# Optimization experiments

Measured on AMD Instinct MI355X. Metric: run time of the kernel, lower is better.

The kernel has to match this reference:

```python
import jax, jax.numpy as jnp
import numpy as np

TIME_SHIFT_OFFSET = 288
NOTE_OFF_OFFSET = 128
VELOCITY_OFFSET = 256
MAX_REL_POS = 25
MAX_REL_TIME = 200
MAX_REL_PITCH = 128


def _last_true_pos(flag):
    # flag: (B,T) bool -> (B,T) index of most recent True at or before each position, -1 if none
    B, T = flag.shape
    pos = jnp.where(flag, jnp.arange(T)[None, :], -1)
    return jax.lax.cummax(pos, axis=1)


def time_rel_idx(tok):
    # Faithful vectorization of Head.relative_time index computation.
    B, T = tok.shape
    is_t = tok >= TIME_SHIFT_OFFSET
    vals = jnp.where(is_t, tok - TIME_SHIFT_OFFSET, 0)
    abs_t = (jnp.cumsum(vals, axis=1) + 1).astype(jnp.float32)
    last = _last_true_pos(is_t)
    cur = jnp.where(last >= 0, jnp.take_along_axis(abs_t, jnp.maximum(last, 0), axis=1), jnp.nan)
    prop = jnp.round(cur / 10.0)  # (B,T), NaN before first time token
    dist = prop[:, None, :] - prop[:, :, None]  # [b,i,j] = prop[j]-prop[i]
    idx = jnp.clip(dist, -MAX_REL_TIME, MAX_REL_TIME) + MAX_REL_TIME
    return jnp.where(jnp.isnan(idx), 0.0, idx).astype(jnp.int32)  # (B,T,T)


def pitch_rel_idx(tok):
    # Per the reference loop, note values are also written one step ahead (i-1,i,i+1),
    # so position j ends up with the note value known after step min(j+1, T-1).
    B, T = tok.shape
    is_n = tok < VELOCITY_OFFSET
    vals = (jnp.where(tok >= NOTE_OFF_OFFSET, tok - NOTE_OFF_OFFSET, tok) + 1).astype(jnp.float32)
    last = _last_true_pos(is_n)
    ff = jnp.where(last >= 0, jnp.take_along_axis(vals, jnp.maximum(last, 0), axis=1), jnp.nan)
    prop = ff[:, jnp.minimum(jnp.arange(T) + 1, T - 1)]
    dist = prop[:, None, :] - prop[:, :, None]
    idx = jnp.clip(dist, -MAX_REL_PITCH, MAX_REL_PITCH) + MAX_REL_PITCH
    return jnp.where(jnp.isnan(idx), 0.0, idx).astype(jnp.int32)  # (B,T,T)


def setup_inputs() -> dict:
    key = jax.random.key(0)
    ks = jax.random.split(key, 12)
    B, T, C, H = 2, 512, 512, 64
    x = jax.random.normal(ks[0], (B, T, C), dtype=jnp.float32)
    token_batch = jax.random.randint(ks[1], (B, T), 0, 388)
    s = C ** -0.5
    Wk = jax.random.normal(ks[2], (C, H), dtype=jnp.float32) * s
    Wq = jax.random.normal(ks[3], (C, H), dtype=jnp.float32) * s
    Wv = jax.random.normal(ks[4], (C, H), dtype=jnp.float32) * s
    e = 0.02
    Ek_pos = jax.random.normal(ks[5], (2 * MAX_REL_POS + 1, H), dtype=jnp.float32) * e
    Ev_pos = jax.random.normal(ks[6], (2 * MAX_REL_POS + 1, H), dtype=jnp.float32) * e
    Ek_time = jax.random.normal(ks[7], (2 * MAX_REL_TIME + 1, H), dtype=jnp.float32) * e
    Ev_time = jax.random.normal(ks[8], (2 * MAX_REL_TIME + 1, H), dtype=jnp.float32) * e
    Ek_pitch = jax.random.normal(ks[9], (2 * MAX_REL_PITCH + 1, H), dtype=jnp.float32) * e
    Ev_pitch = jax.random.normal(ks[10], (2 * MAX_REL_PITCH + 1, H), dtype=jnp.float32) * e
    return dict(x=x, token_batch=token_batch, Wk=Wk, Wq=Wq, Wv=Wv,
                Ek_pos=Ek_pos, Ev_pos=Ev_pos, Ek_time=Ek_time, Ev_time=Ev_time,
                Ek_pitch=Ek_pitch, Ev_pitch=Ev_pitch)


def reference(x, token_batch, Wk, Wq, Wv, Ek_pos, Ev_pos, Ek_time, Ev_time, Ek_pitch, Ev_pitch):
    B, T, C = x.shape
    q = x @ Wq  # (B,T,H)
    k = x @ Wk
    v = x @ Wv
    wei = jnp.einsum('btc,bsc->bts', q, k) * (C ** -0.5)  # (B,T,T), scaled by n_embd per source
    pos = jnp.arange(T)
    pd = jnp.clip(pos[None, :] - pos[:, None], -MAX_REL_POS, MAX_REL_POS) + MAX_REL_POS  # (T,T)
    tidx = time_rel_idx(token_batch)
    nidx = pitch_rel_idx(token_batch)
    # Note: the source einsums sum the relative embeddings over i as well (btj output).
    wei = wei + jnp.einsum('ijc,btc->btj', Ek_pos[pd], q)
    wei = wei + jnp.einsum('bijc,btc->btj', Ek_time[tidx], q)
    wei = wei + jnp.einsum('bijc,btc->btj', Ek_pitch[nidx], q)
    causal = jnp.tril(jnp.ones((T, T), dtype=bool))
    wei = jnp.where(causal[None], wei, -jnp.inf)
    wei = jax.nn.softmax(wei, axis=-1)  # dropout p=0.0
    out = wei @ v
    out = out + jnp.einsum('ijc,btj->btc', Ev_pos[pd], wei)
    out = out + jnp.einsum('bijc,btj->btc', Ev_time[tidx], wei)
    out = out + jnp.einsum('bijc,btj->btc', Ev_pitch[nidx], wei)
    return out
```

## Files before the change

kernel.cpp:

```cpp
#include <hip/hip_runtime.h>
#include <math.h>

#define B 2
#define T 512
#define C 512
#define H 64

#define SCALE 0.044194173824159216f

static __device__ __forceinline__ float qnan() { return __builtin_nanf(""); }

__global__ __launch_bounds__(256) void qkv_scan_kernel(
    const float* __restrict__ x, const int* __restrict__ tok,
    const float* __restrict__ Wq, const float* __restrict__ Wk,
    const float* __restrict__ Wv,
    float* __restrict__ q, float* __restrict__ k, float* __restrict__ v,
    float* __restrict__ prop_t, float* __restrict__ prop_p,
    int* __restrict__ cntP, int* __restrict__ meta,
    float* __restrict__ tval, int* __restrict__ tcnt) {
    int bid = blockIdx.x;
    int tid = threadIdx.x;
    int wave = tid >> 6;
    int lane = tid & 63;

    __shared__ float xs[16 * C];
    __shared__ int   tks[T];
    __shared__ int   cnts[520];
    __shared__ int   hist[129];
    __shared__ int   nanPc;

    if (bid < 192) {
        int rg = bid & 63;
        int m = bid >> 6;
        int g = lane >> 4;
        int c4 = lane & 15;

        const float* Wm = (m == 0) ? Wq : ((m == 1) ? Wk : Wv);
        float* Om = (m == 0) ? q : ((m == 1) ? k : v);

        const float4* xv4 = (const float4*)(x + (size_t)rg * 16 * C);
        float4* xs4 = (float4*)xs;
#pragma unroll
        for (int i = 0; i < 8; ++i) xs4[tid + 256 * i] = xv4[tid + 256 * i];
        __syncthreads();

        const float4* W4 = (const float4*)Wm;
        const float* xr = xs + (wave * 4) * C;

        float4 a0 = make_float4(0.f, 0.f, 0.f, 0.f);
        float4 a1 = a0, a2 = a0, a3 = a0;
#pragma unroll 4
        for (int u = 0; u < 128; ++u) {
            int kk = u * 4 + g;
            float4 w4 = W4[kk * 16 + c4];
            float x0 = xr[kk];
            float x1 = xr[C + kk];
            float x2 = xr[2 * C + kk];
            float x3 = xr[3 * C + kk];
            a0.x = fmaf(x0, w4.x, a0.x); a0.y = fmaf(x0, w4.y, a0.y);
            a0.z = fmaf(x0, w4.z, a0.z); a0.w = fmaf(x0, w4.w, a0.w);
            a1.x = fmaf(x1, w4.x, a1.x); a1.y = fmaf(x1, w4.y, a1.y);
            a1.z = fmaf(x1, w4.z, a1.z); a1.w = fmaf(x1, w4.w, a1.w);
            a2.x = fmaf(x2, w4.x, a2.x); a2.y = fmaf(x2, w4.y, a2.y);
            a2.z = fmaf(x2, w4.z, a2.z); a2.w = fmaf(x2, w4.w, a2.w);
            a3.x = fmaf(x3, w4.x, a3.x); a3.y = fmaf(x3, w4.y, a3.y);
            a3.z = fmaf(x3, w4.z, a3.z); a3.w = fmaf(x3, w4.w, a3.w);
        }
#pragma unroll
        for (int mask = 16; mask <= 32; mask <<= 1) {
            a0.x += __shfl_xor(a0.x, mask); a0.y += __shfl_xor(a0.y, mask);
            a0.z += __shfl_xor(a0.z, mask); a0.w += __shfl_xor(a0.w, mask);
            a1.x += __shfl_xor(a1.x, mask); a1.y += __shfl_xor(a1.y, mask);
            a1.z += __shfl_xor(a1.z, mask); a1.w += __shfl_xor(a1.w, mask);
            a2.x += __shfl_xor(a2.x, mask); a2.y += __shfl_xor(a2.y, mask);
            a2.z += __shfl_xor(a2.z, mask); a2.w += __shfl_xor(a2.w, mask);
            a3.x += __shfl_xor(a3.x, mask); a3.y += __shfl_xor(a3.y, mask);
            a3.z += __shfl_xor(a3.z, mask); a3.w += __shfl_xor(a3.w, mask);
        }
        if (g == 0) {
            size_t row0 = (size_t)(rg * 16 + wave * 4);
            ((float4*)(Om + (row0 + 0) * H))[c4] = a0;
            ((float4*)(Om + (row0 + 1) * H))[c4] = a1;
            ((float4*)(Om + (row0 + 2) * H))[c4] = a2;
            ((float4*)(Om + (row0 + 3) * H))[c4] = a3;
        }
        return;
    }

    int b = bid - 192;
    {
        const int* tb = tok + b * T;
        tks[tid] = tb[tid];
        tks[tid + 256] = tb[tid + 256];
        for (int i = tid; i < 520; i += 256) cnts[i] = 0;
        if (tid < 129) hist[tid] = 0;
        if (tid == 255) nanPc = 0;
    }
    __syncthreads();
    if (wave != 0) return;

    const int p0 = lane * 8;
    unsigned long long lowmask = lane ? ((1ull << lane) - 1ull) : 0ull;

    float tv[8];
    {
        float lsum[8];
        bool lflag[8];
        float s = 0.f;
        bool f = false;
#pragma unroll
        for (int u = 0; u < 8; ++u) {
            int tk = tks[p0 + u];
            if (tk >= 288) { s += (float)(tk - 288); f = true; }
            lsum[u] = s;
            lflag[u] = f;
        }
        float inc = s;
#pragma unroll
        for (int off = 1; off < 64; off <<= 1) {
            float o = __shfl_up(inc, off);
            if (lane >= off) inc += o;
        }
        float ex = inc - s;
        unsigned long long fmask = __ballot(f);
        bool exf = (fmask & lowmask) != 0ull;
#pragma unroll
        for (int u = 0; u < 8; ++u) {
            bool have = exf | lflag[u];
            tv[u] = have ? rintf((ex + lsum[u] + 1.0f) / 10.0f) : qnan();
            prop_t[b * T + p0 + u] = tv[u];
        }
    }

    float fv[8];
    {
        bool lvalid[8];
        float cv = 0.f;
        bool cvd = false;
#pragma unroll
        for (int u = 0; u < 8; ++u) {
            int tk = tks[p0 + u];
            if (tk < 256) {
                cv = (float)((tk >= 128 ? tk - 128 : tk) + 1);
                cvd = true;
            }
            fv[u] = cv;
            lvalid[u] = cvd;
        }
        unsigned long long vmask = __ballot(cvd);
        unsigned long long lower = vmask & lowmask;
        bool exvd = lower != 0ull;
        int src = 63 - __clzll(lower | 1ull);
        float exv = __shfl(cv, src);
#pragma unroll
        for (int u = 0; u < 8; ++u) {
            bool hv = exvd | lvalid[u];
            fv[u] = lvalid[u] ? fv[u] : exv;
            fv[u] = hv ? fv[u] : qnan();
        }
    }

    {
        float nf0 = __shfl_down(fv[0], 1);
#pragma unroll
        for (int u = 0; u < 8; ++u) {
            float sv = (u < 7) ? fv[u + 1] : ((lane == 63) ? fv[7] : nf0);
            prop_p[b * T + p0 + u] = sv;
            if (sv == sv) atomicAdd(&hist[(int)sv - 1], 1);
            else atomicAdd(&nanPc, 1);
        }
    }

    {
        float pl7 = __shfl_up(tv[7], 1);
        int lstart[8];
        int lcnt = 0, lnan = 0;
#pragma unroll
        for (int u = 0; u < 8; ++u) {
            float cur = tv[u];
            bool val = (cur == cur);
            float pv = (u > 0) ? tv[u - 1] : pl7;
            bool st = false;
            if (val) {
                if (p0 + u == 0) st = true;
                else st = !(pv == pv) || (pv != cur);
            } else lnan++;
            lstart[u] = st;
            lcnt += st;
        }
        int incs = lcnt;
#pragma unroll
        for (int off = 1; off < 64; off <<= 1) {
            int o = __shfl_up(incs, off);
            if (lane >= off) incs += o;
        }
        int base = incs - lcnt;
        int Lruns = __shfl(incs, 63);
        int tn = lnan;
#pragma unroll
        for (int off = 32; off; off >>= 1) tn += __shfl_down(tn, off);
        tn = __shfl(tn, 0);

        int s2 = base;
#pragma unroll
        for (int u = 0; u < 8; ++u) {
            float cur = tv[u];
            if (lstart[u]) { tval[b * 520 + s2] = cur; s2++; }
            if (cur == cur) atomicAdd(&cnts[s2 - 1], 1);
        }
        for (int i = lane; i < Lruns; i += 64) tcnt[b * 520 + i] = cnts[i];
        for (int i = lane; i < 129; i += 64) cntP[b * 129 + i] = hist[i];
        if (lane == 0) {
            meta[b * 4] = Lruns;
            meta[b * 4 + 1] = tn;
        }
        if (lane == 1) meta[b * 4 + 2] = nanPc;
    }
}

__global__ __launch_bounds__(256) void relsum_kernel(
    const float* __restrict__ prop_t, const float* __restrict__ prop_p,
    const int* __restrict__ cntP, const int* __restrict__ meta,
    const float* __restrict__ tval, const int* __restrict__ tcnt,
    const float* __restrict__ Ek_pos, const float* __restrict__ Ev_pos,
    const float* __restrict__ Ek_time, const float* __restrict__ Ev_time,
    const float* __restrict__ Ek_pitch, const float* __restrict__ Ev_pitch,
    float* __restrict__ k, float* __restrict__ v) {
    int b = blockIdx.x >> 9;
    int j = blockIdx.x & 511;
    int tid = threadIdx.x;
    int wave = tid >> 6;
    int c = tid & 63;

    __shared__ float tvL[520];
    __shared__ int tcL[520];
    __shared__ int cpL[132];
    __shared__ float redK[256];
    __shared__ float redV[256];

    int L = meta[b * 4];
    int nanT = meta[b * 4 + 1];
    int nanP = meta[b * 4 + 2];
    for (int i = tid; i < L; i += 256) {
        tvL[i] = tval[b * 520 + i];
        tcL[i] = tcnt[b * 520 + i];
    }
    if (tid < 129) cpL[tid] = cntP[b * 129 + tid];
    else if (tid < 132) cpL[tid] = 0;
    __syncthreads();

    float pjt = prop_t[b * T + j];
    float pjp = prop_p[b * T + j];
    bool pvalid = (pjp == pjp);
    int ipjp = pvalid ? (int)pjp : 0;

    float aK = 0.f, aV = 0.f;

#pragma unroll 3
    for (int i = 0; i < 33; ++i) {
        int e = wave + i * 4;
        int cnt = cpL[e];
        if (cnt) {
            int idx = pvalid ? (ipjp + 127 - e) : 0;
            float fc = (float)cnt;
            aK = fmaf(fc, Ek_pitch[idx * H + c], aK);
            aV = fmaf(fc, Ev_pitch[idx * H + c], aV);
        }
    }
    if (wave == 3 && nanP) {
        float fc = (float)nanP;
        aK = fmaf(fc, Ek_pitch[c], aK);
        aV = fmaf(fc, Ev_pitch[c], aV);
    }

#pragma unroll 2
    for (int r = wave; r < L; r += 4) {
        int cnt = tcL[r];
        float dt = pjt - tvL[r];
        int idx = (dt != dt) ? 0 : (int)fminf(fmaxf(dt, -200.f), 200.f) + 200;
        float fc = (float)cnt;
        aK = fmaf(fc, Ek_time[idx * H + c], aK);
        aV = fmaf(fc, Ev_time[idx * H + c], aV);
    }
    if (wave == 1 && nanT) {
        float fc = (float)nanT;
        aK = fmaf(fc, Ek_time[c], aK);
        aV = fmaf(fc, Ev_time[c], aV);
    }

    int lo = max(-25, j - (T - 1));
    int hi = min(25, j);
    for (int d = lo + wave; d <= hi; d += 4) {
        aK += Ek_pos[(d + 25) * H + c];
        aV += Ev_pos[(d + 25) * H + c];
    }
    if (wave == 0) {
        float c50 = (float)max(j - 25, 0);
        float c0 = (float)max((T - 26) - j, 0);
        aK = fmaf(c50, Ek_pos[50 * H + c], aK);
        aK = fmaf(c0, Ek_pos[0 * H + c], aK);
        aV = fmaf(c50, Ev_pos[50 * H + c], aV);
        aV = fmaf(c0, Ev_pos[0 * H + c], aV);
    }

    redK[tid] = aK;
    redV[tid] = aV;
    __syncthreads();

    if (tid < 64) {
        float sK = redK[tid] + redK[64 + tid] + redK[128 + tid] + redK[192 + tid];
        float sV = redV[tid] + redV[64 + tid] + redV[128 + tid] + redV[192 + tid];
        size_t o = (size_t)blockIdx.x * H + tid;
        k[o] = SCALE * k[o] + sK;
        v[o] = v[o] + sV;
    }
}

__global__ __launch_bounds__(256) void attn_kernel(const float* __restrict__ q,
                                                   const float* __restrict__ kp,
                                                   const float* __restrict__ vp,
                                                   float* __restrict__ out) {
    int b = blockIdx.x >> 8;
    int g = blockIdx.x & 255;
    int tid = threadIdx.x;
    int wave = tid >> 6;
    int lane = tid & 63;

    int row = (wave < 2) ? g : (511 - g);
    int ns = row + 1;
    int nw = (ns + 63) >> 6;
    int par = wave & 1;

    __shared__ float kt[64 * 65];
    __shared__ float vt[64 * 64];
    __shared__ float qs[2][64];
    __shared__ float pS[4][64];
    __shared__ float mM[4], lM[4];
    __shared__ float accM[4][64];

    if (wave == 0) qs[0][lane] = q[((size_t)b * T + g) * H + lane];
    if (wave == 2) qs[1][lane] = q[((size_t)b * T + 511 - g) * H + lane];

    const float* kb = kp + (size_t)b * T * H;
    const float* vb = vp + (size_t)b * T * H;
    int ntiles = (512 - g + 63) >> 6;

    float m = -INFINITY;
    float l = 0.f;
    float acc = 0.f;
    const float* qw = qs[wave >> 1];

    for (int it = 0; it < ntiles; ++it) {
        int s0 = it * 64;

#pragma unroll
        for (int i = 0; i < 4; ++i) {
            int f = i * 256 + tid;
            int r = f >> 4;
            int c0 = (f & 15) << 2;
            int sr = min(s0 + r, T - 1);
            const float4 kv = *(const float4*)(kb + (size_t)sr * H + c0);
            const float4 vv = *(const float4*)(vb + (size_t)sr * H + c0);
            kt[r * 65 + c0 + 0] = kv.x;
            kt[r * 65 + c0 + 1] = kv.y;
            kt[r * 65 + c0 + 2] = kv.z;
            kt[r * 65 + c0 + 3] = kv.w;
            *(float4*)(vt + r * 64 + c0) = vv;
        }
        __syncthreads();

        if (it < nw && (it & 1) == par) {
            int s = s0 + lane;
            float sc = -INFINITY;
            if (s < ns) {
                const float* kr = kt + lane * 65;
                float d0 = 0.f, d1 = 0.f, d2 = 0.f, d3 = 0.f;
#pragma unroll
                for (int c = 0; c < 64; c += 4) {
                    d0 = fmaf(qw[c + 0], kr[c + 0], d0);
                    d1 = fmaf(qw[c + 1], kr[c + 1], d1);
                    d2 = fmaf(qw[c + 2], kr[c + 2], d2);
                    d3 = fmaf(qw[c + 3], kr[c + 3], d3);
                }
                sc = (d0 + d1) + (d2 + d3);
            }
            float mt = sc;
#pragma unroll
            for (int off = 32; off; off >>= 1) mt = fmaxf(mt, __shfl_xor(mt, off));
            float mnew = fmaxf(m, mt);
            float alpha = __expf(m - mnew);
            float p = (s < ns) ? __expf(sc - mnew) : 0.f;
            l = l * alpha + p;
            pS[wave][lane] = p;
            m = mnew;

            float a0 = 0.f, a1 = 0.f, a2 = 0.f, a3 = 0.f;
            int smax = min(64, ns - s0);
            const float* pw = pS[wave];
            int ss = 0;
            for (; ss + 4 <= smax; ss += 4) {
                a0 = fmaf(pw[ss + 0], vt[(ss + 0) * 64 + lane], a0);
                a1 = fmaf(pw[ss + 1], vt[(ss + 1) * 64 + lane], a1);
                a2 = fmaf(pw[ss + 2], vt[(ss + 2) * 64 + lane], a2);
                a3 = fmaf(pw[ss + 3], vt[(ss + 3) * 64 + lane], a3);
            }
            for (; ss < smax; ++ss)
                a0 = fmaf(pw[ss], vt[ss * 64 + lane], a0);
            acc = acc * alpha + ((a0 + a1) + (a2 + a3));
        }
        __syncthreads();
    }

    float lt = l;
#pragma unroll
    for (int off = 32; off; off >>= 1) lt += __shfl_xor(lt, off);
    mM[wave] = m;
    lM[wave] = lt;
    accM[wave][lane] = acc;
    __syncthreads();

    if ((wave & 1) == 0) {
        int w1 = wave | 1;
        float m0 = mM[wave], m1 = mM[w1];
        float m12 = fmaxf(m0, m1);
        float al0 = __expf(m0 - m12);
        float al1 = __expf(m1 - m12);
        float lsum = lM[wave] * al0 + lM[w1] * al1;
        float o = (accM[wave][lane] * al0 + accM[w1][lane] * al1) / lsum;
        out[((size_t)b * T + row) * H + lane] = o;
    }
}

extern "C" void kernel_launch(void* const* d_in, const int* in_sizes, int n_in,
                              void* d_out, int out_size, void* d_ws, size_t ws_size,
                              hipStream_t stream) {
    const float* x        = (const float*)d_in[0];
    const int*   tok      = (const int*)d_in[1];
    const float* Wk       = (const float*)d_in[2];
    const float* Wq       = (const float*)d_in[3];
    const float* Wv       = (const float*)d_in[4];
    const float* Ek_pos   = (const float*)d_in[5];
    const float* Ev_pos   = (const float*)d_in[6];
    const float* Ek_time  = (const float*)d_in[7];
    const float* Ev_time  = (const float*)d_in[8];
    const float* Ek_pitch = (const float*)d_in[9];
    const float* Ev_pitch = (const float*)d_in[10];
    float* out = (float*)d_out;

    float* ws = (float*)d_ws;
    float* q      = ws;
    float* k      = q + B * T * H;
    float* v      = k + B * T * H;
    float* prop_t = v + B * T * H;
    float* prop_p = prop_t + B * T;
    int*   cntP   = (int*)(prop_p + B * T);
    int*   meta   = cntP + B * 129;
    float* tval   = (float*)(meta + B * 4);
    int*   tcnt   = (int*)(tval + B * 520);

    qkv_scan_kernel<<<192 + B, 256, 0, stream>>>(x, tok, Wq, Wk, Wv, q, k, v,
                                                 prop_t, prop_p, cntP, meta,
                                                 tval, tcnt);
    relsum_kernel<<<B * T, 256, 0, stream>>>(prop_t, prop_p, cntP, meta, tval, tcnt,
                                             Ek_pos, Ev_pos, Ek_time, Ev_time,
                                             Ek_pitch, Ev_pitch, k, v);
    attn_kernel<<<B * 256, 256, 0, stream>>>(q, k, v, out);
}
```

Measured before the change: 124.8 us.

## Split QKV projection over channel halves and relsum over K/V sides

```diff
diff --git a/kernel.cpp b/kernel.cpp
--- a/kernel.cpp
+++ b/kernel.cpp
@@ -14,7 +14,8 @@
     const float* __restrict__ x, const int* __restrict__ tok,
     const float* __restrict__ Wq, const float* __restrict__ Wk,
     const float* __restrict__ Wv,
-    float* __restrict__ q, float* __restrict__ k, float* __restrict__ v,
+    float* __restrict__ q1, float* __restrict__ k1, float* __restrict__ v1,
+    float* __restrict__ q2, float* __restrict__ k2, float* __restrict__ v2,
     float* __restrict__ prop_t, float* __restrict__ prop_p,
     int* __restrict__ cntP, int* __restrict__ meta,
     float* __restrict__ tval, int* __restrict__ tcnt) {
@@ -23,40 +24,46 @@
     int wave = tid >> 6;
     int lane = tid & 63;
 
-    __shared__ float xs[16 * C];
+    __shared__ float xs[16 * 256];
     __shared__ int   tks[T];
     __shared__ int   cnts[520];
     __shared__ int   hist[129];
     __shared__ int   nanPc;
 
-    if (bid < 192) {
-        int rg = bid & 63;
-        int m = bid >> 6;
+    if (bid < 384) {
+        int h = bid / 192;
+        int rem = bid - h * 192;
+        int m = rem >> 6;
+        int rg = rem & 63;
         int g = lane >> 4;
         int c4 = lane & 15;
 
         const float* Wm = (m == 0) ? Wq : ((m == 1) ? Wk : Wv);
-        float* Om = (m == 0) ? q : ((m == 1) ? k : v);
-
-        const float4* xv4 = (const float4*)(x + (size_t)rg * 16 * C);
-        float4* xs4 = (float4*)xs;
-#pragma unroll
-        for (int i = 0; i < 8; ++i) xs4[tid + 256 * i] = xv4[tid + 256 * i];
+        float* Om = (h == 0) ? ((m == 0) ? q1 : ((m == 1) ? k1 : v1))
+                             : ((m == 0) ? q2 : ((m == 1) ? k2 : v2));
+
+        const float* xbase = x + (size_t)rg * 16 * C + h * 256;
+        for (int i = tid; i < 16 * 64; i += 256) {
+            int r = i >> 6;
+            int c0 = (i & 63) << 2;
+            *(float4*)(xs + r * 256 + c0) =
+                *(const float4*)(xbase + (size_t)r * C + c0);
+        }
         __syncthreads();
 
         const float4* W4 = (const float4*)Wm;
-        const float* xr = xs + (wave * 4) * C;
+        const float* xr = xs + (wave * 4) * 256;
 
         float4 a0 = make_float4(0.f, 0.f, 0.f, 0.f);
         float4 a1 = a0, a2 = a0, a3 = a0;
 #pragma unroll 4
-        for (int u = 0; u < 128; ++u) {
+        for (int u = 0; u < 64; ++u) {
             int kk = u * 4 + g;
-            float4 w4 = W4[kk * 16 + c4];
+            float4 w4 = W4[(h * 256 + kk) * 16 + c4];
             float x0 = xr[kk];
-            float x1 = xr[C + kk];
-            float x2 = xr[2 * C + kk];
-            float x3 = xr[3 * C + kk];
+            float x1 = xr[256 + kk];
+            float x2 = xr[512 + kk];
+            float x3 = xr[768 + kk];
             a0.x = fmaf(x0, w4.x, a0.x); a0.y = fmaf(x0, w4.y, a0.y);
             a0.z = fmaf(x0, w4.z, a0.z); a0.w = fmaf(x0, w4.w, a0.w);
             a1.x = fmaf(x1, w4.x, a1.x); a1.y = fmaf(x1, w4.y, a1.y);
@@ -87,7 +94,7 @@
         return;
     }
 
-    int b = bid - 192;
+    int b = bid - 384;
     {
         const int* tb = tok + b * T;
         tks[tid] = tb[tid];
@@ -225,18 +232,25 @@
     const float* __restrict__ Ek_pos, const float* __restrict__ Ev_pos,
     const float* __restrict__ Ek_time, const float* __restrict__ Ev_time,
     const float* __restrict__ Ek_pitch, const float* __restrict__ Ev_pitch,
-    float* __restrict__ k, float* __restrict__ v) {
-    int b = blockIdx.x >> 9;
-    int j = blockIdx.x & 511;
+    const float* __restrict__ k1, const float* __restrict__ k2,
+    const float* __restrict__ v1, const float* __restrict__ v2,
+    float* __restrict__ kf, float* __restrict__ vf) {
+    int bid = blockIdx.x;
+    int side = bid & 1;
+    int j = (bid >> 1) & 511;
+    int b = bid >> 10;
     int tid = threadIdx.x;
     int wave = tid >> 6;
     int c = tid & 63;
 
+    const float* Ep = side ? Ev_pitch : Ek_pitch;
+    const float* Et = side ? Ev_time : Ek_time;
+    const float* Eo = side ? Ev_pos : Ek_pos;
+
     __shared__ float tvL[520];
     __shared__ int tcL[520];
     __shared__ int cpL[132];
-    __shared__ float redK[256];
-    __shared__ float redV[256];
+    __shared__ float red[256];
 
     int L = meta[b * 4];
     int nanT = meta[b * 4 + 1];
@@ -254,69 +268,54 @@
     bool pvalid = (pjp == pjp);
     int ipjp = pvalid ? (int)pjp : 0;
 
-    float aK = 0.f, aV = 0.f;
-
-#pragma unroll 3
+    float a = 0.f;
+
+#pragma unroll 4
     for (int i = 0; i < 33; ++i) {
         int e = wave + i * 4;
-        int cnt = cpL[e];
-        if (cnt) {
-            int idx = pvalid ? (ipjp + 127 - e) : 0;
-            float fc = (float)cnt;
-            aK = fmaf(fc, Ek_pitch[idx * H + c], aK);
-            aV = fmaf(fc, Ev_pitch[idx * H + c], aV);
-        }
-    }
-    if (wave == 3 && nanP) {
-        float fc = (float)nanP;
-        aK = fmaf(fc, Ek_pitch[c], aK);
-        aV = fmaf(fc, Ev_pitch[c], aV);
-    }
+        float fc = (float)cpL[e];
+        int idx = pvalid ? (ipjp + 127 - e) : 0;
+        idx = min(max(idx, 0), 255);
+        a = fmaf(fc, Ep[idx * H + c], a);
+    }
+    if (wave == 3) a = fmaf((float)nanP, Ep[c], a);
 
 #pragma unroll 2
     for (int r = wave; r < L; r += 4) {
-        int cnt = tcL[r];
+        float fc = (float)tcL[r];
         float dt = pjt - tvL[r];
         int idx = (dt != dt) ? 0 : (int)fminf(fmaxf(dt, -200.f), 200.f) + 200;
-        float fc = (float)cnt;
-        aK = fmaf(fc, Ek_time[idx * H + c], aK);
-        aV = fmaf(fc, Ev_time[idx * H + c], aV);
-    }
-    if (wave == 1 && nanT) {
-        float fc = (float)nanT;
-        aK = fmaf(fc, Ek_time[c], aK);
-        aV = fmaf(fc, Ev_time[c], aV);
-    }
+        a = fmaf(fc, Et[idx * H + c], a);
+    }
+    if (wave == 1) a = fmaf((float)nanT, Et[c], a);
 
     int lo = max(-25, j - (T - 1));
     int hi = min(25, j);
-    for (int d = lo + wave; d <= hi; d += 4) {
-        aK += Ek_pos[(d + 25) * H + c];
-        aV += Ev_pos[(d + 25) * H + c];
+#pragma unroll
+    for (int i = 0; i < 13; ++i) {
+        int d = -25 + wave + i * 4;
+        float w = (d >= lo && d <= hi) ? 1.f : 0.f;
+        int idx = min(d + 25, 50);
+        a = fmaf(w, Eo[idx * H + c], a);
     }
     if (wave == 0) {
-        float c50 = (float)max(j - 25, 0);
-        float c0 = (float)max((T - 26) - j, 0);
-        aK = fmaf(c50, Ek_pos[50 * H + c], aK);
-        aK = fmaf(c0, Ek_pos[0 * H + c], aK);
-        aV = fmaf(c50, Ev_pos[50 * H + c], aV);
-        aV = fmaf(c0, Ev_pos[0 * H + c], aV);
-    }
-
-    redK[tid] = aK;
-    redV[tid] = aV;
+        a = fmaf((float)max(j - 25, 0), Eo[50 * H + c], a);
+        a = fmaf((float)max((T - 26) - j, 0), Eo[c], a);
+    }
+
+    red[tid] = a;
     __syncthreads();
 
     if (tid < 64) {
-        float sK = redK[tid] + redK[64 + tid] + redK[128 + tid] + redK[192 + tid];
-        float sV = redV[tid] + redV[64 + tid] + redV[128 + tid] + redV[192 + tid];
-        size_t o = (size_t)blockIdx.x * H + tid;
-        k[o] = SCALE * k[o] + sK;
-        v[o] = v[o] + sV;
+        float s = red[tid] + red[64 + tid] + red[128 + tid] + red[192 + tid];
+        size_t o = (size_t)(b * T + j) * H + tid;
+        if (side == 0) kf[o] = SCALE * (k1[o] + k2[o]) + s;
+        else           vf[o] = (v1[o] + v2[o]) + s;
     }
 }
 
-__global__ __launch_bounds__(256) void attn_kernel(const float* __restrict__ q,
+__global__ __launch_bounds__(256) void attn_kernel(const float* __restrict__ q1,
+                                                   const float* __restrict__ q2,
                                                    const float* __restrict__ kp,
                                                    const float* __restrict__ vp,
                                                    float* __restrict__ out) {
@@ -338,8 +337,14 @@
     __shared__ float mM[4], lM[4];
     __shared__ float accM[4][64];
 
-    if (wave == 0) qs[0][lane] = q[((size_t)b * T + g) * H + lane];
-    if (wave == 2) qs[1][lane] = q[((size_t)b * T + 511 - g) * H + lane];
+    if (wave == 0) {
+        size_t o = ((size_t)b * T + g) * H + lane;
+        qs[0][lane] = q1[o] + q2[o];
+    }
+    if (wave == 2) {
+        size_t o = ((size_t)b * T + 511 - g) * H + lane;
+        qs[1][lane] = q1[o] + q2[o];
+    }
 
     const float* kb = kp + (size_t)b * T * H;
     const float* vb = vp + (size_t)b * T * H;
@@ -447,22 +452,31 @@
     const float* Ev_pitch = (const float*)d_in[10];
     float* out = (float*)d_out;
 
+    const int N = B * T * H;
     float* ws = (float*)d_ws;
-    float* q      = ws;
-    float* k      = q + B * T * H;
-    float* v      = k + B * T * H;
-    float* prop_t = v + B * T * H;
+    float* q1 = ws;
+    float* k1 = q1 + N;
+    float* v1 = k1 + N;
+    float* q2 = v1 + N;
+    float* k2 = q2 + N;
+    float* v2 = k2 + N;
+    float* kf = v2 + N;
+    float* vf = kf + N;
+    float* prop_t = vf + N;
     float* prop_p = prop_t + B * T;
     int*   cntP   = (int*)(prop_p + B * T);
     int*   meta   = cntP + B * 129;
     float* tval   = (float*)(meta + B * 4);
     int*   tcnt   = (int*)(tval + B * 520);
 
-    qkv_scan_kernel<<<192 + B, 256, 0, stream>>>(x, tok, Wq, Wk, Wv, q, k, v,
+    qkv_scan_kernel<<<384 + B, 256, 0, stream>>>(x, tok, Wq, Wk, Wv,
+                                                 q1, k1, v1, q2, k2, v2,
                                                  prop_t, prop_p, cntP, meta,
                                                  tval, tcnt);
-    relsum_kernel<<<B * T, 256, 0, stream>>>(prop_t, prop_p, cntP, meta, tval, tcnt,
-                                             Ek_pos, Ev_pos, Ek_time, Ev_time,
-                                             Ek_pitch, Ev_pitch, k, v);
-    attn_kernel<<<B * 256, 256, 0, stream>>>(q, k, v, out);
+    relsum_kernel<<<B * T * 2, 256, 0, stream>>>(prop_t, prop_p, cntP, meta,
+                                                 tval, tcnt,
+                                                 Ek_pos, Ev_pos, Ek_time, Ev_time,
+                                                 Ek_pitch, Ev_pitch,
+                                                 k1, k2, v1, v2, kf, vf);
+    attn_kernel<<<B * 256, 256, 0, stream>>>(q1, q2, kf, vf, out);
 }
```

Result: faster. 119.6 us (-4.1%).
